# Kernel optimization log

Measured on AMD Instinct MI355X. Metric: run time of the kernel, lower is better.

Reference implementation:

```python
import jax, jax.numpy as jnp
import numpy as np

WEIGHT = 1000.0      # start/end cell penalty
LONELY_W = 15.0      # cell lit outside cluster
CLUSTER_W = 5.0      # cell unlit inside cluster
CELL_W = 20.0        # cell on a shortest manhattan path
CSIZE_W = 12.0       # cluster-size penalty
GAP_W = 300.0        # gap-to-endpoint penalty
H = W = 10


def _md(y1, x1, y2, x2):
    return jnp.abs(y1 - y2) + jnp.abs(x1 - x2)


def _per_sample(result, points):
    # result: [H, W] float, points: [2, 2] int (row, col) of start and end
    p0y, p0x = points[0, 0], points[0, 1]
    p1y, p1x = points[1, 0], points[1, 1]
    base = _md(p0y, p0x, p1y, p1x)

    loss_start = (2.0 - (result[p0y, p0x] + result[p1y, p1x])) * WEIGHT

    # 8-connected flood fill from start over cells whose value rounds to 1.
    mask = jnp.round(result) == 1.0
    seed = jnp.zeros((H, W), bool).at[p0y, p0x].set(True)

    def dilate(_, c):
        p = jnp.pad(c, 1)
        nb = (p[:-2, :-2] | p[:-2, 1:-1] | p[:-2, 2:] |
              p[1:-1, :-2] | p[1:-1, 2:] |
              p[2:, :-2] | p[2:, 1:-1] | p[2:, 2:])
        return c | (nb & mask)

    # 8-connected diameter of a 10x10 grid is 9; H+W iterations is a safe bound.
    cluster = jax.lax.fori_loop(0, H + W, dilate, seed)

    rows = jnp.arange(H)[:, None]
    cols = jnp.arange(W)[None, :]

    # per-cell manhattan detour penalty
    d2 = _md(rows, cols, p0y, p0x) + _md(rows, cols, p1y, p1x)
    delta = (d2 - base).astype(result.dtype)
    single_cell = jnp.sum(jnp.where(delta == 0.0,
                                    (1.0 - result) * CELL_W,
                                    result * delta * 0.5))

    # NB: the original tests [column, row] membership against [row, col]
    # cluster entries -> transposed membership map. Faithfully reproduced.
    in_cl = cluster.T
    csize = jnp.sum(cluster).astype(result.dtype)
    lonelyness = jnp.sum(jnp.where(in_cl, (1.0 - result) * CLUSTER_W,
                                   result * LONELY_W))
    cluster_size_pen = jnp.sum(jnp.where(in_cl, result * csize * CSIZE_W, 0.0))

    # nearest cluster cell to the end point (strict improvement over base)
    dist_end = _md(rows, cols, p1y, p1x)
    masked = jnp.where(cluster, dist_end, H * W + 10).reshape(-1)
    idx = jnp.argmin(masked)
    minval = masked[idx]
    better = minval < base
    ny = jnp.where(better, idx // W, p0y)
    nx = jnp.where(better, idx % W, p0x)
    gap = jnp.minimum(base, minval)

    oy = p1y - ny
    ox = p1x - nx

    def upd(cond, cy, cx, st):
        by, bx, bg = st
        d = _md(cy, cx, p1y, p1x)
        b = cond & (d < bg)
        return (jnp.where(b, cy, by), jnp.where(b, cx, bx), jnp.where(b, d, bg))

    st = (ny, nx, gap)
    c = ox < 0
    st = upd(c, ny, nx - 1, st)
    st = upd(c & (ny != 0), ny - 1, nx - 1, st)
    st = upd(c & (ny != H - 1), ny + 1, nx - 1, st)
    c = ox > 0
    st = upd(c, ny, nx + 1, st)
    st = upd(c & (ny != 0), ny - 1, nx + 1, st)
    st = upd(c & (ny != H - 1), ny + 1, nx + 1, st)
    st = upd(oy < 0, ny - 1, nx, st)
    st = upd(oy > 0, ny + 1, nx, st)
    ncy = jnp.clip(st[0], 0, H - 1)
    ncx = jnp.clip(st[1], 0, W - 1)

    gap_pen = gap.astype(result.dtype) * GAP_W * (1.0 - result[ncy, ncx])

    return loss_start + lonelyness + single_cell + cluster_size_pen + gap_pen


def setup_inputs() -> dict:
    key = jax.random.key(0)
    k1, k2 = jax.random.split(key)
    B = 262144
    result_given = jax.random.uniform(k1, (B, 1, H, W), dtype=jnp.float32)
    points_given = jax.random.randint(k2, (B, 2, 2), 0, 10, dtype=jnp.int64 if jax.config.jax_enable_x64 else jnp.int32)
    return {"result_given": result_given, "points_given": points_given}


def reference(result_given, points_given):
    losses = jax.vmap(_per_sample)(result_given[:, 0], points_given)
    return jnp.sum(losses).reshape(1)
```

## Files before the change

kernel.cpp:

```cpp
#include <hip/hip_runtime.h>
#include <cstdint>

#define GH 10
#define GW 10

__global__ __launch_bounds__(256, 3) void custom_loss_kernel(
    const float* __restrict__ result,
    const int* __restrict__ points,
    float* __restrict__ out,
    int B)
{
    __shared__ float lds[128 * 100];
    const int tix = threadIdx.x;

    {
        const size_t base4 = (size_t)blockIdx.x * (128 * 25);
        const size_t total4 = (size_t)B * 25;
        float4* lds4 = (float4*)lds;
        const float4* g4 = (const float4*)result;
#pragma unroll
        for (int k = 0; k < 12; ++k) {
            const int off = k * 256 + tix;
            if (base4 + off < total4) lds4[off] = g4[base4 + off];
        }
        const int off = 12 * 256 + tix;
        if (tix < 128 && base4 + off < total4) lds4[off] = g4[base4 + off];
    }
    __syncthreads();

    const int s_local = tix >> 1;
    const int h = tix & 1;
    const int s = blockIdx.x * 128 + s_local;
    float loss = 0.f;
    if (s < B) {
        const float* __restrict__ sp = lds + s_local * 100;
        const int4 p = ((const int4*)points)[s];
        const int p0y = p.x, p0x = p.y, p1y = p.z, p1x = p.w;
        const int dy0 = abs(p0y - p1y), dx0 = abs(p0x - p1x);
        const int base0 = dy0 + dx0;
        const int idx0 = p0y * GW + p0x;
        const int idx1 = p1y * GW + p1x;
        const float rs = sp[idx0];
        const float re = sp[idx1];

        float adxf[10], inboxf[10];
#pragma unroll
        for (int x = 0; x < 10; ++x) {
            const int a = abs(x - p0x) + abs(x - p1x) - dx0;
            adxf[x] = (float)a;
            inboxf[x] = (a == 0) ? 1.f : 0.f;
        }

        const float2* rp2 = (const float2*)(sp + h * 50);
        float vv[50];
#pragma unroll
        for (int i = 0; i < 25; ++i) {
            const float2 t = rp2[i];
            vv[2 * i] = t.x; vv[2 * i + 1] = t.y;
        }

        float sum_h = 0.f, sc_h = 0.f, box_h = 0.f;
        uint64_t mword = 0;
#pragma unroll
        for (int i = 0; i < 5; ++i) {
            const int y = 5 * h + i;
            const float* v = vv + 10 * i;
            const float rowacc = ((v[0]+v[1])+(v[2]+v[3])) +
                                 ((v[4]+v[5])+(v[6]+v[7])) + (v[8]+v[9]);
            sum_h += rowacc;
            const int ay = abs(y - p0y) + abs(y - p1y) - dy0;
            sc_h = fmaf((float)ay, rowacc, sc_h);
            float boxrow = 0.f;
            uint32_t rm = 0u;
#pragma unroll
            for (int x = 0; x < 10; ++x) {
                sc_h = fmaf(adxf[x], v[x], sc_h);
                boxrow = fmaf(inboxf[x], v[x], boxrow);
                rm |= (v[x] > 0.5f) ? (1u << x) : 0u;
            }
            box_h += (ay == 0) ? boxrow : 0.f;
            mword |= (uint64_t)rm << (10 * i);
        }
        const float sum_all = sum_h + __shfl_xor(sum_h, 1);
        const float sc      = sc_h  + __shfl_xor(sc_h, 1);
        const float boxSum  = box_h + __shfl_xor(box_h, 1);
        const uint64_t mo = (uint64_t)__shfl_xor((unsigned long long)mword, 1);
        const uint64_t mlo = h ? mo : mword;
        const uint64_t mhi = h ? mword : mo;

        const uint64_t M50 = (1ull << 50) - 1;
        const uint64_t C0  = 0x10040100401ull;
        const uint64_t NC0 = M50 & ~C0;
        const uint64_t NC9 = M50 & ~(C0 << 9);
        uint64_t clo = 0, chi = 0;
        if (idx0 < 50) clo = 1ull << idx0; else chi = 1ull << (idx0 - 50);
#pragma unroll 1
        for (int it = 0; it < GH + GW; ++it) {
            const uint64_t hlo = clo | ((clo << 1) & NC0) | ((clo >> 1) & NC9);
            const uint64_t hhi = chi | ((chi << 1) & NC0) | ((chi >> 1) & NC9);
            uint64_t nlo = (hlo | (hlo << 10) | (hlo >> 10) | ((hhi & 0x3FFull) << 40)) & mlo;
            uint64_t nhi = (hhi | (hhi << 10) | (hhi >> 10) | (hlo >> 40)) & mhi;
            nlo |= clo; nhi |= chi;
            if (nlo == clo && nhi == chi) break;
            clo = nlo; chi = nhi;
        }
        const int K = __popcll(clo) + __popcll(chi);

        const uint64_t wlo = clo >> (5 * h);
        const uint64_t whi = chi >> (5 * h);
        float st_h = 0.f;
#pragma unroll
        for (int i = 0; i < 5; ++i) {
            const float* v = vv + 10 * i;
#pragma unroll
            for (int x = 0; x < 10; ++x) {
                const uint64_t w = (x < 5) ? wlo : whi;
                const uint32_t bit = (uint32_t)((w >> ((x % 5) * 10 + i)) & 1ull);
                st_h = fmaf((float)bit, v[x], st_h);
            }
        }
        const float S_T = st_h + __shfl_xor(st_h, 1);

        int bestd = 1000, bidx = 0;
        const uint64_t cw = h ? chi : clo;
#pragma unroll
        for (int i = 0; i < 5; ++i) {
            const int y = 5 * h + i;
            const uint32_t rb = (uint32_t)((cw >> (10 * i)) & 0x3FFull);
            const uint32_t left  = rb & ((2u << p1x) - 1);
            const uint32_t right = rb >> p1x;
            const int dl = left  ? (p1x - (31 - __builtin_clz(left))) : 1000;
            const int dr = right ? __builtin_ctz(right) : 1000;
            int dx, xx;
            if (dl <= dr) { dx = dl; xx = p1x - dl; }
            else          { dx = dr; xx = p1x + dr; }
            const int d = abs(y - p1y) + dx;
            if (rb && d < bestd) { bestd = d; bidx = y * GW + xx; }
        }
        {
            const int od = __shfl_xor(bestd, 1);
            const int oi = __shfl_xor(bidx, 1);
            if (od < bestd || (od == bestd && oi < bidx)) { bestd = od; bidx = oi; }
        }

        const bool better = bestd < base0;
        const int ny = better ? bidx / 10 : p0y;
        const int nx = better ? bidx % 10 : p0x;
        const int gap = min(base0, bestd);

        int by = ny, bx = nx, bg = gap;
        const int oy = p1y - ny, ox = p1x - nx;
        auto upd = [&](bool cond, int cy, int cx) {
            const int d = abs(cy - p1y) + abs(cx - p1x);
            if (cond && (d < bg)) { by = cy; bx = cx; bg = d; }
        };
        upd(ox < 0,                     ny,     nx - 1);
        upd((ox < 0) && (ny != 0),      ny - 1, nx - 1);
        upd((ox < 0) && (ny != GH - 1), ny + 1, nx - 1);
        upd(ox > 0,                     ny,     nx + 1);
        upd((ox > 0) && (ny != 0),      ny - 1, nx + 1);
        upd((ox > 0) && (ny != GH - 1), ny + 1, nx + 1);
        upd(oy < 0,                     ny - 1, nx);
        upd(oy > 0,                     ny + 1, nx);
        const int ncy = min(max(by, 0), GH - 1);
        const int ncx = min(max(bx, 0), GW - 1);
        const float rn = sp[ncy * GW + ncx];

        const float csf = (float)K;
        const float nboxf = (float)((dy0 + 1) * (dx0 + 1));
        const float loss_start = (2.f - (rs + re)) * 1000.f;
        const float lon = 5.f * csf + 15.f * sum_all - 20.f * S_T;
        const float single_cell = 0.5f * sc + 20.f * (nboxf - boxSum);
        const float cpen = 12.f * csf * S_T;
        const float gap_pen = (float)gap * 300.f * (1.f - rn);
        loss = loss_start + lon + single_cell + cpen + gap_pen;
        if (h != 0) loss = 0.f;
    }

#pragma unroll
    for (int off = 32; off > 0; off >>= 1)
        loss += __shfl_down(loss, off);
    __shared__ float wsum[4];
    const int lane = threadIdx.x & 63;
    const int wid = threadIdx.x >> 6;
    if (lane == 0) wsum[wid] = loss;
    __syncthreads();
    if (threadIdx.x == 0)
        atomicAdd(out, wsum[0] + wsum[1] + wsum[2] + wsum[3]);
}

extern "C" void kernel_launch(void* const* d_in, const int* in_sizes, int n_in,
                              void* d_out, int out_size, void* d_ws, size_t ws_size,
                              hipStream_t stream)
{
    const float* result = (const float*)d_in[0];
    const int* points   = (const int*)d_in[1];
    float* out = (float*)d_out;
    const int B = in_sizes[0] / 100;
    hipMemsetAsync(out, 0, sizeof(float), stream);
    const int block = 256;
    const int grid = (2 * B + block - 1) / block;
    custom_loss_kernel<<<grid, block, 0, stream>>>(result, points, out, B);
}
```

Measured before the change: 180.4 us.

## Stage input through small LDS chunks per wavefront to raise occupancy

Shrinks the shared staging buffer from 128 to 32 samples and loads the block's data in four chunks. After each chunk, only the owning wavefront copies its samples into registers. The smaller LDS footprint lets launch bounds rise to 6 blocks per CU, aimed at hiding memory latency. The cost is extra barriers that serialize the loads, plus one global re-read for the gap-cell value, and the higher occupancy target may force register spills given the 50-float per-thread array.

```diff
diff --git a/kernel.cpp b/kernel.cpp
--- a/kernel.cpp
+++ b/kernel.cpp
@@ -4,44 +4,67 @@
 #define GH 10
 #define GW 10
 
-__global__ __launch_bounds__(256, 3) void custom_loss_kernel(
+__global__ __launch_bounds__(256, 6) void custom_loss_kernel(
     const float* __restrict__ result,
     const int* __restrict__ points,
     float* __restrict__ out,
     int B)
 {
-    __shared__ float lds[128 * 100];
+    __shared__ float lds[32 * 100];
+    __shared__ float wsum[4];
     const int tix = threadIdx.x;
+    const int lane = tix & 63;
+    const int wid = tix >> 6;
+
+    const int s_local = tix >> 1;
+    const int h = tix & 1;
+    const int s = blockIdx.x * 128 + s_local;
+
+    int p0y = 0, p0x = 0, p1y = 0, p1x = 0;
+    if (s < B) {
+        const int4 p = ((const int4*)points)[s];
+        p0y = p.x; p0x = p.y; p1y = p.z; p1x = p.w;
+    }
+    const int idx0 = p0y * GW + p0x;
+    const int idx1 = p1y * GW + p1x;
+
+    float vv[50];
+    float rs = 0.f, re = 0.f;
 
     {
-        const size_t base4 = (size_t)blockIdx.x * (128 * 25);
         const size_t total4 = (size_t)B * 25;
         float4* lds4 = (float4*)lds;
         const float4* g4 = (const float4*)result;
 #pragma unroll
-        for (int k = 0; k < 12; ++k) {
-            const int off = k * 256 + tix;
-            if (base4 + off < total4) lds4[off] = g4[base4 + off];
-        }
-        const int off = 12 * 256 + tix;
-        if (tix < 128 && base4 + off < total4) lds4[off] = g4[base4 + off];
+        for (int c = 0; c < 4; ++c) {
+            const size_t base4 = (size_t)blockIdx.x * 3200 + c * 800;
+#pragma unroll
+            for (int k = 0; k < 3; ++k) {
+                const int off = k * 256 + tix;
+                if (base4 + off < total4) lds4[off] = g4[base4 + off];
+            }
+            const int off = 768 + tix;
+            if (tix < 32 && base4 + off < total4) lds4[off] = g4[base4 + off];
+            __syncthreads();
+            if (wid == c && s < B) {
+                const float* __restrict__ sp = lds + (lane >> 1) * 100;
+                rs = sp[idx0];
+                re = sp[idx1];
+                const float2* rp2 = (const float2*)(sp + h * 50);
+#pragma unroll
+                for (int i = 0; i < 25; ++i) {
+                    const float2 t = rp2[i];
+                    vv[2 * i] = t.x; vv[2 * i + 1] = t.y;
+                }
+            }
+            __syncthreads();
+        }
     }
-    __syncthreads();
-
-    const int s_local = tix >> 1;
-    const int h = tix & 1;
-    const int s = blockIdx.x * 128 + s_local;
+
     float loss = 0.f;
     if (s < B) {
-        const float* __restrict__ sp = lds + s_local * 100;
-        const int4 p = ((const int4*)points)[s];
-        const int p0y = p.x, p0x = p.y, p1y = p.z, p1x = p.w;
         const int dy0 = abs(p0y - p1y), dx0 = abs(p0x - p1x);
         const int base0 = dy0 + dx0;
-        const int idx0 = p0y * GW + p0x;
-        const int idx1 = p1y * GW + p1x;
-        const float rs = sp[idx0];
-        const float re = sp[idx1];
 
         float adxf[10], inboxf[10];
 #pragma unroll
@@ -49,14 +72,6 @@
             const int a = abs(x - p0x) + abs(x - p1x) - dx0;
             adxf[x] = (float)a;
             inboxf[x] = (a == 0) ? 1.f : 0.f;
-        }
-
-        const float2* rp2 = (const float2*)(sp + h * 50);
-        float vv[50];
-#pragma unroll
-        for (int i = 0; i < 25; ++i) {
-            const float2 t = rp2[i];
-            vv[2 * i] = t.x; vv[2 * i + 1] = t.y;
         }
 
         float sum_h = 0.f, sc_h = 0.f, box_h = 0.f;
@@ -164,7 +179,7 @@
         upd(oy > 0,                     ny + 1, nx);
         const int ncy = min(max(by, 0), GH - 1);
         const int ncx = min(max(bx, 0), GW - 1);
-        const float rn = sp[ncy * GW + ncx];
+        const float rn = result[(size_t)s * 100 + ncy * GW + ncx];
 
         const float csf = (float)K;
         const float nboxf = (float)((dy0 + 1) * (dx0 + 1));
@@ -180,12 +195,9 @@
 #pragma unroll
     for (int off = 32; off > 0; off >>= 1)
         loss += __shfl_down(loss, off);
-    __shared__ float wsum[4];
-    const int lane = threadIdx.x & 63;
-    const int wid = threadIdx.x >> 6;
     if (lane == 0) wsum[wid] = loss;
     __syncthreads();
-    if (threadIdx.x == 0)
+    if (tix == 0)
         atomicAdd(out, wsum[0] + wsum[1] + wsum[2] + wsum[3]);
 }
 
```

Measured after the change: 208.0 us. +15.3%, slower.
